# Performance work log

Hardware: AMD Instinct MI355X
Metric: run time of the kernel (lower is better)

Reference implementation:

```python
import jax, jax.numpy as jnp
import numpy as np
import math

EPS = 1e-5

def conv1x1(x, w):
    # x: (B,C,H,W), w: (O,C)
    return jnp.einsum('bchw,oc->bohw', x, w)

def bn(x, gamma, beta, mean, var):
    # inference-mode batchnorm, params shape (C,)
    s = (gamma / jnp.sqrt(var + EPS))[None, :, None, None]
    b = (beta - mean * gamma / jnp.sqrt(var + EPS))[None, :, None, None]
    return x * s + b

def setup_inputs() -> dict:
    key = jax.random.key(0)
    ks = jax.random.split(key, 16)
    B, C1, C2, OUT, W, H = 4, 256, 64, 64, 64, 64
    inp = {
        'rgb': jax.random.normal(ks[0], (B, C2, W, H), jnp.float32),
        'dep': jax.random.normal(ks[1], (B, C1, W, H), jnp.float32),
        # dep fusion conv (1x1) + BN
        'conv_w': jax.random.normal(ks[2], (C2, C1), jnp.float32) * (1.0 / np.sqrt(C1)),
        'bn1_g': jax.random.uniform(ks[3], (C2,), jnp.float32, 0.5, 1.5),
        'bn1_b': jax.random.normal(ks[4], (C2,), jnp.float32) * 0.1,
        'bn1_m': jax.random.normal(ks[5], (C2,), jnp.float32) * 0.1,
        'bn1_v': jax.random.uniform(ks[6], (C2,), jnp.float32, 0.5, 1.5),
        # attention projections (1x1, no bias)
        'rgb_w': jax.random.normal(ks[7], (C2, C2), jnp.float32) * (1.0 / np.sqrt(C2)),
        'dep_w': jax.random.normal(ks[8], (C2, C2), jnp.float32) * (1.0 / np.sqrt(C2)),
        # mlp: ConvBNReLU(C2,24,1) then ConvBNSig(24,OUT,1)
        'mlp1_w': jax.random.normal(ks[9], (24, C2), jnp.float32) * (1.0 / np.sqrt(C2)),
        'bn2_g': jax.random.uniform(ks[10], (24,), jnp.float32, 0.5, 1.5),
        'bn2_b': jax.random.normal(ks[11], (24,), jnp.float32) * 0.1,
        'bn2_m': jax.random.normal(ks[12], (24,), jnp.float32) * 0.1,
        'bn2_v': jax.random.uniform(ks[13], (24,), jnp.float32, 0.5, 1.5),
        'mlp2_w': jax.random.normal(ks[14], (OUT, 24), jnp.float32) * (1.0 / np.sqrt(24)),
        'bn3_g': jax.random.uniform(jax.random.fold_in(key, 20), (OUT,), jnp.float32, 0.5, 1.5),
        'bn3_b': jax.random.normal(jax.random.fold_in(key, 21), (OUT,), jnp.float32) * 0.1,
        'bn3_m': jax.random.normal(jax.random.fold_in(key, 22), (OUT,), jnp.float32) * 0.1,
        'bn3_v': jax.random.uniform(jax.random.fold_in(key, 23), (OUT,), jnp.float32, 0.5, 1.5),
    }
    return inp

def reference(rgb, dep, conv_w, bn1_g, bn1_b, bn1_m, bn1_v, rgb_w, dep_w,
              mlp1_w, bn2_g, bn2_b, bn2_m, bn2_v, mlp2_w, bn3_g, bn3_b, bn3_m, bn3_v):
    # dep = ConvBNReLU(dep)
    dep = jax.nn.relu(bn(conv1x1(dep, conv_w), bn1_g, bn1_b, bn1_m, bn1_v))
    rgbd = rgb + dep
    B, C, W, H = rgb.shape
    N = W * H
    proj_rgb = conv1x1(rgb, rgb_w).reshape(B, C, N)  # (B,C,N)
    proj_dep = conv1x1(dep, dep_w).reshape(B, C, N)  # (B,C,N)
    # energy[b,i,j] = <proj_rgb[:,i], proj_dep[:,j]> / sqrt(C)
    energy = jnp.einsum('bci,bcj->bij', proj_rgb, proj_dep) / math.sqrt(C)
    attn = jax.nn.softmax(energy, axis=1)  # torch Softmax(dim=1): over rows i
    att_r = jnp.einsum('bci,bij->bcj', proj_rgb, attn)
    att_b = jnp.einsum('bci,bij->bcj', proj_dep, attn)
    output = (att_r + att_b).reshape(B, C, W, H) + rgbd
    gap = output.mean(axis=(2, 3), keepdims=True)  # (B,C,1,1)
    h = jax.nn.relu(bn(conv1x1(gap, mlp1_w), bn2_g, bn2_b, bn2_m, bn2_v))
    gate = jax.nn.sigmoid(bn(conv1x1(h, mlp2_w), bn3_g, bn3_b, bn3_m, bn3_v))
    return gate
```

## Files before the change

### kernel.cpp

```cpp
#include <hip/hip_runtime.h>
#include <hip/hip_bf16.h>


typedef __bf16 bf16;
typedef __bf16 bf16x4 __attribute__((ext_vector_type(4)));
typedef __bf16 bf16x8 __attribute__((ext_vector_type(8)));
typedef float  f32x4  __attribute__((ext_vector_type(4)));
typedef float  float4v __attribute__((ext_vector_type(4)));
typedef short  s4     __attribute__((ext_vector_type(4)));

#define MFMA_BF16(a, b, c) __builtin_amdgcn_mfma_f32_16x16x32_bf16((a), (b), (c), 0, 0, 0)

#if defined(__has_builtin)
# if __has_builtin(__builtin_amdgcn_mfma_f32_16x16x16bf16_1k)
#  define MFMA16_BUILTIN(a, b, c) __builtin_amdgcn_mfma_f32_16x16x16bf16_1k((a), (b), (c), 0, 0, 0)
# elif __has_builtin(__builtin_amdgcn_mfma_f32_16x16x16_bf16)
#  define MFMA16_BUILTIN(a, b, c) __builtin_amdgcn_mfma_f32_16x16x16_bf16((a), (b), (c), 0, 0, 0)
# endif
#endif

__device__ __forceinline__ f32x4 MFMA16(s4 a, s4 b, f32x4 c) {
#ifdef MFMA16_BUILTIN
    return MFMA16_BUILTIN(a, b, c);
#else
    asm("v_mfma_f32_16x16x16_bf16 %0, %1, %2, %0" : "+v"(c) : "v"(a), "v"(b));
    return c;
#endif
}

#if defined(__has_builtin)
# if __has_builtin(__builtin_amdgcn_exp2f)
#  define EXP2(x) __builtin_amdgcn_exp2f(x)
# else
#  define EXP2(x) exp2f(x)
# endif
#else
# define EXP2(x) exp2f(x)
#endif

#define K_E 0.18033688f

__device__ __forceinline__ int swz128(int row, int colByte) {
    return row * 128 + (colByte ^ ((row & 7) << 4));
}
__device__ __forceinline__ int swz512(int row, int colByte) {
    return row * 512 + (colByte ^ ((row & 15) << 4));
}

#define OW_W   0
#define OW_WR  32768
#define OW_WD  40960
#define OT_C   0
#define OT_R   16384
#define OT_D   20480
#define O_S1   49152
#define O_B1   49408
#define O_RED  49664
#define SMEMA  51712

__global__ __launch_bounds__(512, 2) void k_front(
    const float* __restrict__ rgb, const float* __restrict__ dep,
    const float* __restrict__ conv_w,
    const float* __restrict__ bn1_g, const float* __restrict__ bn1_b,
    const float* __restrict__ bn1_m, const float* __restrict__ bn1_v,
    const float* __restrict__ rgb_w, const float* __restrict__ dep_w,
    bf16* __restrict__ prF, bf16* __restrict__ pdF, bf16* __restrict__ pvF,
    float* __restrict__ rgbdPart, int* __restrict__ counter)
{
    const int bid = blockIdx.x;
    const int xcd = bid & 7;
    const int b    = xcd >> 1;
    const int tile = ((bid >> 3) << 1) | (xcd & 1);
    const int p0   = tile * 32;
    const int tid = threadIdx.x;
    const int w   = tid >> 6;
    const int lane = tid & 63;
    const int l15 = lane & 15;
    const int lg  = lane >> 4;
    const int ot4 = w & 3;
    const int ot  = ot4 * 16;
    const int ph  = w >> 2;

    if (bid == 0 && tid == 0) *counter = 0;

    __shared__ __align__(16) unsigned char smem[SMEMA];
    float* s1 = (float*)(smem + O_S1);
    float* b1 = (float*)(smem + O_B1);
    float* red = (float*)(smem + O_RED);

    {
        unsigned char* ldsW  = smem + OW_W;
        unsigned char* ldsWR = smem + OW_WR;
        unsigned char* ldsWD = smem + OW_WD;
        #pragma unroll
        for (int q = 0; q < 8; ++q) {
            const int idx = (q * 512 + tid) * 4;
            float4v v = *(const float4v*)(conv_w + idx);
            const int o = idx >> 8, c = idx & 255;
            bf16x4 h;
            #pragma unroll
            for (int j = 0; j < 4; ++j) h[j] = (bf16)v[j];
            *(bf16x4*)(ldsW + swz512(o, c * 2)) = h;
        }
        #pragma unroll
        for (int q = 0; q < 2; ++q) {
            const int idx = (q * 512 + tid) * 4;
            const int o = idx >> 6, c = idx & 63;
            float4v v = *(const float4v*)(rgb_w + idx);
            bf16x4 h;
            #pragma unroll
            for (int j = 0; j < 4; ++j) h[j] = (bf16)v[j];
            *(bf16x4*)(ldsWR + swz128(o, c * 2)) = h;
            v = *(const float4v*)(dep_w + idx);
            #pragma unroll
            for (int j = 0; j < 4; ++j) h[j] = (bf16)v[j];
            *(bf16x4*)(ldsWD + swz128(o, c * 2)) = h;
        }
        if (tid < 64) {
            float sc = bn1_g[tid] * rsqrtf(bn1_v[tid] + 1e-5f);
            s1[tid] = sc;
            b1[tid] = bn1_b[tid] - bn1_m[tid] * sc;
        }
    }
    __syncthreads();

    bf16x8 aW[8], aR[2], aD[2];
    {
        const unsigned char* ldsW  = smem + OW_W;
        const unsigned char* ldsWR = smem + OW_WR;
        const unsigned char* ldsWD = smem + OW_WD;
        const int row = ot + l15;
        #pragma unroll
        for (int kk = 0; kk < 8; ++kk)
            aW[kk] = *(const bf16x8*)(ldsW + swz512(row, (kk * 32 + lg * 8) * 2));
        #pragma unroll
        for (int kk = 0; kk < 2; ++kk) {
            aR[kk] = *(const bf16x8*)(ldsWR + swz128(row, (kk * 32 + lg * 8) * 2));
            aD[kk] = *(const bf16x8*)(ldsWD + swz128(row, (kk * 32 + lg * 8) * 2));
        }
    }
    __syncthreads();

    unsigned char* ldsC = smem + OT_C;
    unsigned char* ldsR = smem + OT_R;
    unsigned char* ldsD = smem + OT_D;
    const float* depb = dep + (size_t)b * 256 * 4096;
    const float* rgbb = rgb + (size_t)b * 64 * 4096;
    {
        const int c0 = tid >> 3, seg = tid & 7;
        #pragma unroll
        for (int r = 0; r < 4; ++r) {
            const int c = r * 64 + c0;
            float4v v = *(const float4v*)(depb + (size_t)c * 4096 + p0 + seg * 4);
            #pragma unroll
            for (int k = 0; k < 4; ++k)
                *(bf16*)(ldsC + swz512(seg * 4 + k, c * 2)) = (bf16)v[k];
        }
        float4v v = *(const float4v*)(rgbb + (size_t)c0 * 4096 + p0 + seg * 4);
        #pragma unroll
        for (int k = 0; k < 4; ++k)
            *(bf16*)(ldsR + swz128(seg * 4 + k, c0 * 2)) = (bf16)v[k];
    }
    __syncthreads();

    const int prow = ph * 16 + l15;
    f32x4 acc = {0.f, 0.f, 0.f, 0.f};
    #pragma unroll
    for (int kk = 0; kk < 8; ++kk) {
        bf16x8 bF = *(const bf16x8*)(ldsC + swz512(prow, (kk * 32 + lg * 8) * 2));
        acc = MFMA_BF16(aW[kk], bF, acc);
    }
    {
        const int o0 = ot + lg * 4;
        bf16x4 v4;
        #pragma unroll
        for (int r = 0; r < 4; ++r) {
            float x = acc[r] * s1[o0 + r] + b1[o0 + r];
            v4[r] = (bf16)(x > 0.f ? x : 0.f);
        }
        *(bf16x4*)(ldsD + swz128(prow, o0 * 2)) = v4;
    }
    __syncthreads();

    f32x4 accR = {0.f, 0.f, 0.f, 0.f}, accD = {0.f, 0.f, 0.f, 0.f};
    #pragma unroll
    for (int kk = 0; kk < 2; ++kk) {
        const int cb = (kk * 32 + lg * 8) * 2;
        bf16x8 bR = *(const bf16x8*)(ldsR + swz128(prow, cb));
        bf16x8 bD = *(const bf16x8*)(ldsD + swz128(prow, cb));
        accR = MFMA_BF16(aR[kk], bR, accR);
        accD = MFMA_BF16(aD[kk], bD, accD);
    }
    {
        const int o0 = ot + lg * 4;
        const size_t itile = (size_t)tile * 2 + ph;
        const size_t fbase = (size_t)b * 262144 + itile * 1024;
        const size_t prOff = fbase + (size_t)(o0 >> 3) * 128 + l15 * 8 + (o0 & 7);
        bf16x4 vR, vD;
        #pragma unroll
        for (int r = 0; r < 4; ++r) {
            vR[r] = (bf16)(accR[r] * K_E);
            vD[r] = (bf16)accD[r];
        }
        *(bf16x4*)(prF + prOff) = vR;
        *(bf16x4*)(pdF + prOff) = vD;
        const size_t pvBase = fbase + ot4 * 256 + (l15 >> 2) * 64 + lg * 16 + (l15 & 3);
        #pragma unroll
        for (int r = 0; r < 4; ++r)
            pvF[pvBase + r * 4] = (bf16)(accR[r] + accD[r]);
    }

    {
        const int c = tid & 63, g8 = tid >> 6;
        float sum = 0.f;
        #pragma unroll
        for (int q = 0; q < 4; ++q) {
            const int pp = g8 * 4 + q;
            sum += (float)*(const bf16*)(ldsR + swz128(pp, c * 2))
                 + (float)*(const bf16*)(ldsD + swz128(pp, c * 2));
        }
        red[g8 * 64 + c] = sum;
    }
    __syncthreads();
    if (tid < 64) {
        float s = 0.f;
        #pragma unroll
        for (int g = 0; g < 8; ++g) s += red[g * 64 + tid];
        rgbdPart[((size_t)b * 128 + tile) * 64 + tid] = s;
    }
}

__global__ __launch_bounds__(512, 2) void k_col(
    const bf16* __restrict__ prF, const bf16* __restrict__ pdF,
    const bf16* __restrict__ pvF,
    float* __restrict__ gapPart, const float* __restrict__ rgbdPart,
    int* __restrict__ counter,
    const float* __restrict__ mlp1_w,
    const float* __restrict__ bn2_g, const float* __restrict__ bn2_b,
    const float* __restrict__ bn2_m, const float* __restrict__ bn2_v,
    const float* __restrict__ mlp2_w,
    const float* __restrict__ bn3_g, const float* __restrict__ bn3_b,
    const float* __restrict__ bn3_m, const float* __restrict__ bn3_v,
    float* __restrict__ out)
{
    const int bid = blockIdx.x;
    const int xcd = bid & 7, b = xcd >> 1;
    const int jt64 = ((bid >> 3) << 1) | (xcd & 1);
    const int tid = threadIdx.x;
    const int ih = tid >> 6, lane = tid & 63;
    const int l15 = lane & 15, lg = lane >> 4;

    __shared__ float zred[8][64];
    __shared__ float zfull[64];
    __shared__ float gred[8][64];
    __shared__ float gv4[4][64];
    __shared__ float h4[4][24];
    __shared__ int winflag;
    if (tid == 0) winflag = 0;

    const bf16* prb = prF + (size_t)b * 262144;
    const bf16* pdb = pdF + (size_t)b * 262144;
    const bf16* pvb = pvF + (size_t)b * 262144;

    bf16x8 B0[4], B1[4];
    #pragma unroll
    for (int jt = 0; jt < 4; ++jt) {
        const bf16* q = pdb + (size_t)(jt64 * 4 + jt) * 1024 + lane * 8;
        B0[jt] = *(const bf16x8*)q;
        B1[jt] = *(const bf16x8*)(q + 512);
    }

    f32x4 acc[4][4];
    #pragma unroll
    for (int jt = 0; jt < 4; ++jt)
        #pragma unroll
        for (int cb = 0; cb < 4; ++cb)
            acc[jt][cb] = (f32x4){0.f, 0.f, 0.f, 0.f};
    float z[4] = {0.f, 0.f, 0.f, 0.f};

    const bf16* pA = prb + (size_t)ih * 32 * 1024;
    const bf16* pV = pvb + (size_t)ih * 32 * 1024;

    bf16x8 a0 = *(const bf16x8*)(pA + lane * 8);
    bf16x8 a1 = *(const bf16x8*)(pA + 512 + lane * 8);
    bf16x4 v0 = *(const bf16x4*)(pV + lane * 4);
    bf16x4 v1 = *(const bf16x4*)(pV + 256 + lane * 4);
    bf16x4 v2 = *(const bf16x4*)(pV + 512 + lane * 4);
    bf16x4 v3 = *(const bf16x4*)(pV + 768 + lane * 4);

    for (int t = 0; t < 32; ++t) {
        const bf16x8 ca0 = a0, ca1 = a1;
        const bf16x4 cv0 = v0, cv1 = v1, cv2 = v2, cv3 = v3;
        if (t < 31) {
            pA += 1024; pV += 1024;
            a0 = *(const bf16x8*)(pA + lane * 8);
            a1 = *(const bf16x8*)(pA + 512 + lane * 8);
            v0 = *(const bf16x4*)(pV + lane * 4);
            v1 = *(const bf16x4*)(pV + 256 + lane * 4);
            v2 = *(const bf16x4*)(pV + 512 + lane * 4);
            v3 = *(const bf16x4*)(pV + 768 + lane * 4);
        }
        #pragma unroll
        for (int jt = 0; jt < 4; ++jt) {
            f32x4 e = {0.f, 0.f, 0.f, 0.f};
            e = MFMA_BF16(ca0, B0[jt], e);
            e = MFMA_BF16(ca1, B1[jt], e);
            bf16x4 ph;
            #pragma unroll
            for (int r = 0; r < 4; ++r) {
                float pf = EXP2(e[r]);
                z[jt] += pf;
                ph[r] = (bf16)pf;
            }
            const s4 pB = __builtin_bit_cast(s4, ph);
            acc[jt][0] = MFMA16(__builtin_bit_cast(s4, cv0), pB, acc[jt][0]);
            acc[jt][1] = MFMA16(__builtin_bit_cast(s4, cv1), pB, acc[jt][1]);
            acc[jt][2] = MFMA16(__builtin_bit_cast(s4, cv2), pB, acc[jt][2]);
            acc[jt][3] = MFMA16(__builtin_bit_cast(s4, cv3), pB, acc[jt][3]);
        }
    }

    #pragma unroll
    for (int jt = 0; jt < 4; ++jt) {
        float zv = z[jt];
        zv += __shfl_xor(zv, 16);
        zv += __shfl_xor(zv, 32);
        if (lane < 16) zred[ih][jt * 16 + lane] = zv;
    }
    __syncthreads();
    if (tid < 64) {
        float s = 0.f;
        #pragma unroll
        for (int k = 0; k < 8; ++k) s += zred[k][tid];
        zfull[tid] = s;
    }
    __syncthreads();

    float zinv[4];
    #pragma unroll
    for (int jt = 0; jt < 4; ++jt) {
        const float zj = zfull[jt * 16 + l15];
        float zi = __builtin_amdgcn_rcpf(zj);
        zinv[jt] = zi * (2.0f - zj * zi);
    }
    #pragma unroll
    for (int cb = 0; cb < 4; ++cb) {
        #pragma unroll
        for (int r = 0; r < 4; ++r) {
            float v = acc[0][cb][r] * zinv[0] + acc[1][cb][r] * zinv[1]
                    + acc[2][cb][r] * zinv[2] + acc[3][cb][r] * zinv[3];
            v += __shfl_xor(v, 1);
            v += __shfl_xor(v, 2);
            v += __shfl_xor(v, 4);
            v += __shfl_xor(v, 8);
            if (l15 == 0) gred[ih][cb * 16 + lg * 4 + r] = v;
        }
    }
    __syncthreads();
    if (tid < 64) {
        float s = 0.f;
        #pragma unroll
        for (int k = 0; k < 8; ++k) s += gred[k][tid];
        gapPart[((size_t)b * 64 + jt64) * 64 + tid] = s;
        __threadfence();
        int old = atomicAdd(counter, 1);
        if (old == 256 * 64 - 1) winflag = 1;
    }
    __syncthreads();

    if (winflag) {
        __threadfence();
        const int wb = ih >> 1, half = ih & 1;
        float acc2 = 0.f;
        const float* gp = gapPart + ((size_t)wb * 64 + half * 32) * 64 + lane;
        #pragma unroll 4
        for (int r = 0; r < 32; ++r) acc2 += gp[r * 64];
        const float* rp = rgbdPart + ((size_t)wb * 128 + half * 64) * 64 + lane;
        #pragma unroll 4
        for (int r = 0; r < 64; ++r) acc2 += rp[r * 64];
        gred[ih][lane] = acc2;
        __syncthreads();
        if (tid < 256) {
            const int b4 = tid >> 6, c = tid & 63;
            gv4[b4][c] = (gred[2 * b4][c] + gred[2 * b4 + 1][c]) * (1.f / 4096.f);
        }
        __syncthreads();
        if (tid < 96) {
            const int b4 = tid / 24, o = tid % 24;
            float a = 0.f;
            #pragma unroll
            for (int cc = 0; cc < 64; ++cc) a += mlp1_w[o * 64 + cc] * gv4[b4][cc];
            float sc = bn2_g[o] * rsqrtf(bn2_v[o] + 1e-5f);
            a = a * sc + bn2_b[o] - bn2_m[o] * sc;
            h4[b4][o] = a > 0.f ? a : 0.f;
        }
        __syncthreads();
        if (tid < 256) {
            const int b4 = tid >> 6, c = tid & 63;
            float u = 0.f;
            #pragma unroll
            for (int o = 0; o < 24; ++o) u += mlp2_w[c * 24 + o] * h4[b4][o];
            float sc = bn3_g[c] * rsqrtf(bn3_v[c] + 1e-5f);
            u = u * sc + bn3_b[c] - bn3_m[c] * sc;
            out[b4 * 64 + c] = 1.f / (1.f + __expf(-u));
        }
    }
}

extern "C" void kernel_launch(void* const* d_in, const int* in_sizes, int n_in,
                              void* d_out, int out_size, void* d_ws, size_t ws_size,
                              hipStream_t stream)
{
    const float* rgb    = (const float*)d_in[0];
    const float* dep    = (const float*)d_in[1];
    const float* conv_w = (const float*)d_in[2];
    const float* bn1_g  = (const float*)d_in[3];
    const float* bn1_b  = (const float*)d_in[4];
    const float* bn1_m  = (const float*)d_in[5];
    const float* bn1_v  = (const float*)d_in[6];
    const float* rgb_w  = (const float*)d_in[7];
    const float* dep_w  = (const float*)d_in[8];
    const float* mlp1_w = (const float*)d_in[9];
    const float* bn2_g  = (const float*)d_in[10];
    const float* bn2_b  = (const float*)d_in[11];
    const float* bn2_m  = (const float*)d_in[12];
    const float* bn2_v  = (const float*)d_in[13];
    const float* mlp2_w = (const float*)d_in[14];
    const float* bn3_g  = (const float*)d_in[15];
    const float* bn3_b  = (const float*)d_in[16];
    const float* bn3_m  = (const float*)d_in[17];
    const float* bn3_v  = (const float*)d_in[18];

    char* ws = (char*)d_ws;
    bf16*  prF      = (bf16*)(ws);
    bf16*  pdF      = (bf16*)(ws + (2u << 20));
    bf16*  pvF      = (bf16*)(ws + (4u << 20));
    float* rgbdPart = (float*)(ws + (6u << 20));
    float* gapPart  = (float*)(ws + (6u << 20) + (128u << 10));
    int*   counter  = (int*)  (ws + (6u << 20) + (192u << 10));

    k_front<<<512, 512, 0, stream>>>(rgb, dep, conv_w,
                                     bn1_g, bn1_b, bn1_m, bn1_v,
                                     rgb_w, dep_w,
                                     prF, pdF, pvF, rgbdPart, counter);
    k_col<<<256, 512, 0, stream>>>(prF, pdF, pvF, gapPart, rgbdPart, counter,
                                   mlp1_w, bn2_g, bn2_b, bn2_m, bn2_v,
                                   mlp2_w, bn3_g, bn3_b, bn3_m, bn3_v,
                                   (float*)d_out);
}
```

Before: 51.95 us.

## Double-buffer k_col row-tile loads and interleave tile order across waves

The k_col main loop now keeps two register sets of A/V operands, so each tile's global loads are issued two iterations ahead instead of one. The tile indexing also changes: each wave used to walk a contiguous block of 32 tiles (ih*32+t) and now takes every eighth tile (t*8+ih), so the eight waves read adjacent tiles at the same time. The aim is to hide global-load latency and improve L2/cache locality across the waves of a block. It costs extra VGPRs under launch_bounds(512,2), which risks spills.

```diff
diff --git a/kernel.cpp b/kernel.cpp
--- a/kernel.cpp
+++ b/kernel.cpp
@@ -230,6 +230,40 @@
     }
 }
 
+#define LOADSET(A0, A1, V0, V1, V2, V3, q)                                    \
+    {                                                                         \
+        const bf16* pA_ = prb + (size_t)((q) * 8 + ih) * 1024;                \
+        const bf16* pV_ = pvb + (size_t)((q) * 8 + ih) * 1024;                \
+        A0 = *(const bf16x8*)(pA_ + lane * 8);                                \
+        A1 = *(const bf16x8*)(pA_ + 512 + lane * 8);                          \
+        V0 = *(const bf16x4*)(pV_ + lane * 4);                                \
+        V1 = *(const bf16x4*)(pV_ + 256 + lane * 4);                          \
+        V2 = *(const bf16x4*)(pV_ + 512 + lane * 4);                          \
+        V3 = *(const bf16x4*)(pV_ + 768 + lane * 4);                          \
+    }
+
+#define COMPUTESET(A0, A1, V0, V1, V2, V3)                                    \
+    {                                                                         \
+        _Pragma("unroll")                                                     \
+        for (int jt = 0; jt < 4; ++jt) {                                      \
+            f32x4 e = {0.f, 0.f, 0.f, 0.f};                                   \
+            e = MFMA_BF16(A0, B0[jt], e);                                     \
+            e = MFMA_BF16(A1, B1[jt], e);                                     \
+            bf16x4 ph_;                                                       \
+            _Pragma("unroll")                                                 \
+            for (int r = 0; r < 4; ++r) {                                     \
+                float pf_ = EXP2(e[r]);                                       \
+                z[jt] += pf_;                                                 \
+                ph_[r] = (bf16)pf_;                                           \
+            }                                                                 \
+            const s4 pB_ = __builtin_bit_cast(s4, ph_);                       \
+            acc[jt][0] = MFMA16(__builtin_bit_cast(s4, V0), pB_, acc[jt][0]); \
+            acc[jt][1] = MFMA16(__builtin_bit_cast(s4, V1), pB_, acc[jt][1]); \
+            acc[jt][2] = MFMA16(__builtin_bit_cast(s4, V2), pB_, acc[jt][2]); \
+            acc[jt][3] = MFMA16(__builtin_bit_cast(s4, V3), pB_, acc[jt][3]); \
+        }                                                                     \
+    }
+
 __global__ __launch_bounds__(512, 2) void k_col(
     const bf16* __restrict__ prF, const bf16* __restrict__ pdF,
     const bf16* __restrict__ pvF,
@@ -278,46 +312,16 @@
             acc[jt][cb] = (f32x4){0.f, 0.f, 0.f, 0.f};
     float z[4] = {0.f, 0.f, 0.f, 0.f};
 
-    const bf16* pA = prb + (size_t)ih * 32 * 1024;
-    const bf16* pV = pvb + (size_t)ih * 32 * 1024;
-
-    bf16x8 a0 = *(const bf16x8*)(pA + lane * 8);
-    bf16x8 a1 = *(const bf16x8*)(pA + 512 + lane * 8);
-    bf16x4 v0 = *(const bf16x4*)(pV + lane * 4);
-    bf16x4 v1 = *(const bf16x4*)(pV + 256 + lane * 4);
-    bf16x4 v2 = *(const bf16x4*)(pV + 512 + lane * 4);
-    bf16x4 v3 = *(const bf16x4*)(pV + 768 + lane * 4);
-
-    for (int t = 0; t < 32; ++t) {
-        const bf16x8 ca0 = a0, ca1 = a1;
-        const bf16x4 cv0 = v0, cv1 = v1, cv2 = v2, cv3 = v3;
-        if (t < 31) {
-            pA += 1024; pV += 1024;
-            a0 = *(const bf16x8*)(pA + lane * 8);
-            a1 = *(const bf16x8*)(pA + 512 + lane * 8);
-            v0 = *(const bf16x4*)(pV + lane * 4);
-            v1 = *(const bf16x4*)(pV + 256 + lane * 4);
-            v2 = *(const bf16x4*)(pV + 512 + lane * 4);
-            v3 = *(const bf16x4*)(pV + 768 + lane * 4);
-        }
-        #pragma unroll
-        for (int jt = 0; jt < 4; ++jt) {
-            f32x4 e = {0.f, 0.f, 0.f, 0.f};
-            e = MFMA_BF16(ca0, B0[jt], e);
-            e = MFMA_BF16(ca1, B1[jt], e);
-            bf16x4 ph;
-            #pragma unroll
-            for (int r = 0; r < 4; ++r) {
-                float pf = EXP2(e[r]);
-                z[jt] += pf;
-                ph[r] = (bf16)pf;
-            }
-            const s4 pB = __builtin_bit_cast(s4, ph);
-            acc[jt][0] = MFMA16(__builtin_bit_cast(s4, cv0), pB, acc[jt][0]);
-            acc[jt][1] = MFMA16(__builtin_bit_cast(s4, cv1), pB, acc[jt][1]);
-            acc[jt][2] = MFMA16(__builtin_bit_cast(s4, cv2), pB, acc[jt][2]);
-            acc[jt][3] = MFMA16(__builtin_bit_cast(s4, cv3), pB, acc[jt][3]);
-        }
+    bf16x8 a0A, a1A, a0B, a1B;
+    bf16x4 v0A, v1A, v2A, v3A, v0B, v1B, v2B, v3B;
+    LOADSET(a0A, a1A, v0A, v1A, v2A, v3A, 0);
+    LOADSET(a0B, a1B, v0B, v1B, v2B, v3B, 1);
+
+    for (int t = 0; t < 32; t += 2) {
+        COMPUTESET(a0A, a1A, v0A, v1A, v2A, v3A);
+        if (t + 2 < 32) LOADSET(a0A, a1A, v0A, v1A, v2A, v3A, t + 2);
+        COMPUTESET(a0B, a1B, v0B, v1B, v2B, v3B);
+        if (t + 3 < 32) LOADSET(a0B, a1B, v0B, v1B, v2B, v3B, t + 3);
     }
 
     #pragma unroll
```

Result: slower. 55.04 us (+6.0%).
